# Kernel optimization log

Hardware: AMD Instinct MI355X
Metric: run time of the kernel (lower is better)

The kernel has to match this reference:

```python
import jax, jax.numpy as jnp
import numpy as np

EPS = 1e-5
NEG_SLOPE = 0.2


def _minmax(a):
    m = jnp.min(a)
    return (a - m) / (jnp.max(a) - m)


def _bn(x2d, gamma, beta):
    # train-mode BatchNorm1d: stats over axis 0 (biased variance)
    mu = x2d.mean(0)
    var = x2d.var(0)
    return gamma * (x2d - mu) * jax.lax.rsqrt(var + EPS) + beta


def _leaky(a):
    return jnp.where(a >= 0, a, NEG_SLOPE * a)


def setup_inputs() -> dict:
    key = jax.random.key(0)
    ks = jax.random.split(key, 10)
    B, C, N = 256, 1024, 80
    stdv = 1.0 / np.sqrt(C)
    return {
        "x": jax.random.normal(ks[0], (B, C, N), jnp.float32),
        "out1": jax.random.normal(ks[1], (B, N), jnp.float32),
        "adj_param": jax.random.uniform(ks[2], (N, N), jnp.float32),
        "static_weight": jax.random.uniform(ks[3], (C, C), jnp.float32, -stdv, stdv),
        "dynamic_weight": jax.random.uniform(ks[4], (C, C), jnp.float32, -stdv, stdv),
        "conv_global_w": jax.random.normal(ks[5], (C, C), jnp.float32) * 0.02,
        "conv_global_b": jnp.zeros((C,), jnp.float32),
        "conv_co_w": jax.random.normal(ks[6], (N, 2 * C), jnp.float32) * 0.02,
        "conv_co_b": jnp.zeros((N,), jnp.float32),
        "bn_gamma": jnp.ones((C,), jnp.float32),
        "bn_beta": jnp.zeros((C,), jnp.float32),
        "bng_gamma": jnp.ones((C,), jnp.float32),
        "bng_beta": jnp.zeros((C,), jnp.float32),
    }


def reference(x, out1, adj_param, static_weight, dynamic_weight,
              conv_global_w, conv_global_b, conv_co_w, conv_co_b,
              bn_gamma, bn_beta, bng_gamma, bng_beta):
    B, C, N = x.shape

    # ---- static GCN ----
    sadj = _minmax(adj_param)                               # (N,N)
    D = jax.lax.rsqrt(sadj.sum(1))                          # A.sum(1)^-0.5
    adj = D[:, None] * sadj.T * D[None, :]                  # gen_adj, diag matmuls as broadcast
    support = jnp.einsum('bcn,co->bno', x, static_weight)   # (B,N,C)
    h = jnp.einsum('nm,bmo->bno', adj, support)             # (B,N,C)
    h = _bn(h.reshape(-1, C), bn_gamma, bn_beta).reshape(B, N, C)
    out_static = _leaky(h).transpose(0, 2, 1)               # (B,C,N)
    x2 = x + out_static

    # ---- dynamic graph construction ----
    glb = x2.mean(2)                                        # GAP over nodes -> (B,C)
    glb = glb @ conv_global_w.T + conv_global_b             # 1x1 conv
    glb = _leaky(_bn(glb, bng_gamma, bng_beta))             # BN over batch (L=1)
    cat = jnp.concatenate([jnp.broadcast_to(glb[:, :, None], (B, C, N)), x2], axis=1)  # (B,2C,N)
    dadj = jnp.einsum('oc,bcn->bon', conv_co_w, cat) + conv_co_b[None, :, None]        # (B,N,N)
    dadj = _minmax(dadj)

    # ---- adjacency loss ----
    t1 = jnp.einsum('bn,bnm->bm', out1, dadj) / N
    loss = jnp.sum(jnp.linalg.norm(out1 - t1, axis=1))
    loss = loss + jnp.sum(jnp.linalg.norm((dadj - sadj).reshape(B, -1), axis=1))

    # ---- dynamic GCN ----
    Dd = jax.lax.rsqrt(dadj.sum(2))                         # (B,N)
    tadj = Dd[:, :, None] * dadj.transpose(0, 2, 1) * Dd[:, None, :]
    sup = jnp.einsum('bcn,co->bno', x2, dynamic_weight)
    h2 = jnp.einsum('bnm,bmo->bno', tadj, sup)
    h2 = _bn(h2.reshape(-1, C), bn_gamma, bn_beta).reshape(B, N, C).transpose(0, 2, 1)
    h2 = _leaky(h2)                                         # (B,C,N)
    return h2, loss
```

## Files before the change

### kernel.cpp

```cpp
#include <hip/hip_runtime.h>
#include <hip/hip_bf16.h>
#include <math.h>

#define TPB 256

constexpr int   B_  = 256;
constexpr int   C_  = 1024;
constexpr int   N_  = 80;
constexpr int   BNr = B_ * N_;
constexpr int   CN  = C_ * N_;
constexpr long  BCN = (long)B_ * C_ * N_;
constexpr int   NN  = N_ * N_;
constexpr int   BNN = B_ * NN;
constexpr float EPSf = 1e-5f;

typedef __bf16 bf16x8 __attribute__((ext_vector_type(8)));
typedef float  f32x4  __attribute__((ext_vector_type(4)));

__device__ __forceinline__ float leakyf(float v) { return v >= 0.0f ? v : 0.2f * v; }

__device__ __forceinline__ ushort f2bf(float f) {
  __hip_bfloat16 h = __float2bfloat16(f);
  ushort u; __builtin_memcpy(&u, &h, 2); return u;
}
__device__ __forceinline__ float b2f(ushort u) {
  __hip_bfloat16 h; __builtin_memcpy(&h, &u, 2);
  return __bfloat162float(h);
}

#define GLOBAL_AS __attribute__((address_space(1)))
#define LDS_AS    __attribute__((address_space(3)))
__device__ __forceinline__ void load_lds16(const void* g, void* l) {
  __builtin_amdgcn_global_load_lds((const GLOBAL_AS void*)g, (LDS_AS void*)l, 16, 0, 0);
}

__global__ __launch_bounds__(256) void k_prep_all(
    const float* __restrict__ Ws, const float* __restrict__ Wd,
    const float* __restrict__ Wco, const float* __restrict__ Wg,
    ushort* __restrict__ Wts, ushort* __restrict__ Wtd,
    ushort* __restrict__ Wco1t, ushort* __restrict__ Wco2t, ushort* __restrict__ Wg_bf,
    float* __restrict__ zbase,
    const float* __restrict__ ap, float* __restrict__ sadj,
    ushort* __restrict__ adj_bf, float* __restrict__ lossa) {
  __shared__ float sh[NN];
  __shared__ float red[TPB];
  __shared__ float sD[N_];
  __shared__ float s_lo, s_hi;
  const int t = threadIdx.x;
  const int blk = blockIdx.x;
  if (blk < 2048) {
    const float* W = (blk < 1024) ? Ws : Wd;
    ushort* Wt = (blk < 1024) ? Wts : Wtd;
    const int bb = blk & 1023;
    const int bx = bb & 31, by = bb >> 5;
    const int tx = t % 32, ty = t / 32;
    const int r0 = by * 32, c0 = bx * 32;
#pragma unroll
    for (int k = 0; k < 4; ++k) sh[(ty + 8 * k) * 33 + tx] = W[(size_t)(r0 + ty + 8 * k) * C_ + c0 + tx];
    __syncthreads();
#pragma unroll
    for (int k = 0; k < 4; ++k) Wt[(size_t)(c0 + ty + 8 * k) * C_ + r0 + tx] = f2bf(sh[tx * 33 + ty + 8 * k]);
  } else if (blk < 2208) {
    const int i4 = ((blk - 2048) * TPB + t) * 4;
    const int o = i4 >> 11, k = i4 & 2047;
    float4 v = *(const float4*)&Wco[(size_t)o * 2048 + k];
    ushort4 u;
    u.x = f2bf(v.x); u.y = f2bf(v.y); u.z = f2bf(v.z); u.w = f2bf(v.w);
    if (k < C_) *(ushort4*)&Wco1t[(size_t)o * C_ + k] = u;
    else        *(ushort4*)&Wco2t[(size_t)o * C_ + (k - C_)] = u;
  } else if (blk < 3232) {
    const long i4 = ((long)(blk - 2208) * TPB + t) * 4;
    float4 v = *(const float4*)&Wg[i4];
    ushort4 u;
    u.x = f2bf(v.x); u.y = f2bf(v.y); u.z = f2bf(v.z); u.w = f2bf(v.w);
    *(ushort4*)&Wg_bf[i4] = u;
  } else if (blk < 3258) {
    const int i = ((blk - 3232) * TPB + t) * 4;
    float4 z = make_float4(0.f, 0.f, 0.f, 0.f);
    *(float4*)&zbase[i] = z;
  } else {
    float lo = 3.4e38f, hi = -3.4e38f;
    for (int i = t; i < NN; i += TPB) { float v = ap[i]; sh[i] = v; lo = fminf(lo, v); hi = fmaxf(hi, v); }
    red[t] = lo; __syncthreads();
    for (int o = 128; o > 0; o >>= 1) { if (t < o) red[t] = fminf(red[t], red[t + o]); __syncthreads(); }
    if (t == 0) s_lo = red[0];
    __syncthreads();
    red[t] = hi; __syncthreads();
    for (int o = 128; o > 0; o >>= 1) { if (t < o) red[t] = fmaxf(red[t], red[t + o]); __syncthreads(); }
    if (t == 0) s_hi = red[0];
    __syncthreads();
    const float inv = 1.0f / (s_hi - s_lo);
    for (int i = t; i < NN; i += TPB) { float v = (sh[i] - s_lo) * inv; sh[i] = v; sadj[i] = v; }
    __syncthreads();
    if (t < N_) { float sum = 0.f; for (int m = 0; m < N_; ++m) sum += sh[t * N_ + m]; sD[t] = rsqrtf(sum); }
    if (t == 0) *lossa = 0.0f;
    __syncthreads();
    for (int i = t; i < N_ * 96; i += TPB) {
      const int n = i / 96, m = i % 96;
      adj_bf[i] = f2bf((m < N_) ? sD[n] * sh[m * N_ + n] * sD[m] : 0.0f);
    }
  }
}

__global__ __launch_bounds__(256) void k_fold_mfma(const float* __restrict__ Xf32,
                                                   const ushort* __restrict__ Xbf,
                                                   const void* __restrict__ adjsrc,
                                                   ushort* __restrict__ outp, int mode,
                                                   const float* __restrict__ bmin,
                                                   const float* __restrict__ bmax) {
  __shared__ __align__(16) ushort sX[128][104];
  __shared__ __align__(16) ushort sAdj[80][104];
  __shared__ float sD[N_];
  __shared__ float rl[TPB], rh[TPB];
  __shared__ float s_lo, s_inv;
  const int t = threadIdx.x;
  const int b  = blockIdx.x >> 3;
  const int c0 = (blockIdx.x & 7) * 128;

  if (mode == 0) {
    const ushort* ab = (const ushort*)adjsrc;
    for (int i = t; i < (N_ * 96) / 4; i += TPB) {
      ushort4 v = *(const ushort4*)&ab[i * 4];
      *(ushort4*)&sAdj[(i * 4) / 96][(i * 4) % 96] = v;
    }
    __syncthreads();
  } else {
    rl[t] = (t < 160) ? bmin[t] : 3.4e38f;
    rh[t] = (t < 160) ? bmax[t] : -3.4e38f;
    __syncthreads();
    for (int o = 128; o > 0; o >>= 1) {
      if (t < o) { rl[t] = fminf(rl[t], rl[t + o]); rh[t] = fmaxf(rh[t], rh[t + o]); }
      __syncthreads();
    }
    if (t == 0) { s_lo = rl[0]; s_inv = 1.0f / (rh[0] - rl[0]); }
    __syncthreads();
    const float lo = s_lo, inv = s_inv;
    float* sF = (float*)&sX[0][0];
    const float* db = (const float*)adjsrc + (size_t)b * NN;
    for (int i = t; i < NN / 4; i += TPB) {
      float4 v = *(const float4*)&db[i * 4];
      v.x = (v.x - lo) * inv; v.y = (v.y - lo) * inv;
      v.z = (v.z - lo) * inv; v.w = (v.w - lo) * inv;
      *(float4*)&sF[i * 4] = v;
    }
    __syncthreads();
    if (t < N_) { float s = 0.f; for (int m = 0; m < N_; ++m) s += sF[t * N_ + m]; sD[t] = rsqrtf(s); }
    __syncthreads();
    for (int i = t; i < N_ * 96; i += TPB) {
      const int n = i / 96, m = i % 96;
      sAdj[n][m] = f2bf((m < N_) ? sF[m * N_ + n] * sD[n] * sD[m] : 0.0f);
    }
    __syncthreads();
  }

  if (mode == 0) {
    const float* Xb = Xf32 + ((size_t)b * C_ + c0) * N_;
    for (int i = t; i < (128 * N_) / 4; i += TPB) {
      float4 v = *(const float4*)&Xb[i * 4];
      const int r = (i * 4) / N_, m = (i * 4) % N_;
      ushort4 u; u.x = f2bf(v.x); u.y = f2bf(v.y); u.z = f2bf(v.z); u.w = f2bf(v.w);
      *(ushort4*)&sX[r][m] = u;
    }
  } else {
    const ushort* Xb = Xbf + ((size_t)b * C_ + c0) * N_;
    for (int i = t; i < (128 * N_) / 8; i += TPB) {
      const int r = i / 10, m = (i % 10) * 8;
      uint4 v = *(const uint4*)&Xb[(size_t)r * N_ + m];
      *(uint4*)&sX[r][m] = v;
    }
  }
  for (int i = t; i < (128 * 16) / 4; i += TPB) {
    const int r = i / 4, m = 80 + (i % 4) * 4;
    ushort4 z; z.x = 0; z.y = 0; z.z = 0; z.w = 0;
    *(ushort4*)&sX[r][m] = z;
  }
  __syncthreads();

  const int lane = t & 63, wid = t >> 6;
  const int l16 = lane & 15, lq = lane >> 4;
  f32x4 acc[2][5];
#pragma unroll
  for (int i = 0; i < 2; ++i)
#pragma unroll
    for (int j = 0; j < 5; ++j) { f32x4 z = {0.f, 0.f, 0.f, 0.f}; acc[i][j] = z; }
  bf16x8 af[2][3], bfr[5][3];
#pragma unroll
  for (int i = 0; i < 2; ++i)
#pragma unroll
    for (int kk = 0; kk < 3; ++kk)
      af[i][kk] = *(const bf16x8*)&sX[wid * 32 + i * 16 + l16][kk * 32 + lq * 8];
#pragma unroll
  for (int j = 0; j < 5; ++j)
#pragma unroll
    for (int kk = 0; kk < 3; ++kk)
      bfr[j][kk] = *(const bf16x8*)&sAdj[j * 16 + l16][kk * 32 + lq * 8];
#pragma unroll
  for (int i = 0; i < 2; ++i)
#pragma unroll
    for (int j = 0; j < 5; ++j)
#pragma unroll
      for (int kk = 0; kk < 3; ++kk)
        acc[i][j] = __builtin_amdgcn_mfma_f32_16x16x32_bf16(af[i][kk], bfr[j][kk], acc[i][j], 0, 0, 0);

  ushort* ob = outp + (size_t)b * CN;
#pragma unroll
  for (int i = 0; i < 2; ++i) {
    const int c = c0 + wid * 32 + i * 16 + lq * 4;
#pragma unroll
    for (int j = 0; j < 5; ++j) {
      const int n = j * 16 + l16;
      ushort4 u;
      u.x = f2bf(acc[i][j][0]); u.y = f2bf(acc[i][j][1]);
      u.z = f2bf(acc[i][j][2]); u.w = f2bf(acc[i][j][3]);
      *(ushort4*)&ob[(size_t)n * C_ + c] = u;
    }
  }
}

__global__ __launch_bounds__(512, 2) void k_gemm_256(const ushort* __restrict__ A,
                                                     const ushort* __restrict__ Bt,
                                                     void* __restrict__ outp, int out_bf,
                                                     float* __restrict__ bnsum,
                                                     float* __restrict__ bnsq) {
  __shared__ ushort sA[2][256 * 64];
  __shared__ ushort sB[2][256 * 64];
  const int t = threadIdx.x;
  const int lane = t & 63, wid = t >> 6;
  const int wm = wid >> 2, wn = wid & 3;
  const int l16 = lane & 15, lq = lane >> 4;

  const int lin = blockIdx.x;
  const int xcd = lin & 7, bi = lin >> 3;
  const int tm = xcd * 10 + (bi >> 2);
  const int tn = bi & 3;
  const int m0 = tm * 256, o0 = tn * 256;

  const int srow = t >> 3;
  const int sswz = ((t & 7) ^ ((t >> 3) & 7)) * 8;

  f32x4 acc[8][4];
#pragma unroll
  for (int i = 0; i < 8; ++i)
#pragma unroll
    for (int j = 0; j < 4; ++j) { f32x4 z = {0.f, 0.f, 0.f, 0.f}; acc[i][j] = z; }

  bf16x8 afr[4][2], bfr0[2][2], bfr1[2][2];

#define STA(PAR, ROWB, KT) load_lds16(A  + (size_t)(m0 + (ROWB) + srow) * C_ + (KT) * 64 + sswz, \
                                      &sA[PAR][((ROWB) + (wid << 3)) * 64])
#define STB(PAR, ROWB, KT) load_lds16(Bt + (size_t)(o0 + (ROWB) + srow) * C_ + (KT) * 64 + sswz, \
                                      &sB[PAR][((ROWB) + (wid << 3)) * 64])
#define STA_H(PAR, H, KT) { STA(PAR, (H)*128, KT); STA(PAR, (H)*128 + 64, KT); }
#define STB_H(PAR, H, KT) { STB(PAR, (H)*128, KT); STB(PAR, (H)*128 + 64, KT); }

#define RDA(PAR, MH)                                                                      \
  _Pragma("unroll") for (int fi = 0; fi < 4; ++fi) {                                      \
    const int row = ((MH) ? 128 : 0) + wm * 64 + fi * 16 + l16;                           \
    _Pragma("unroll") for (int kk = 0; kk < 2; ++kk)                                      \
      afr[fi][kk] = *(const bf16x8*)&sA[PAR][row * 64 + ((kk * 4 + lq) ^ (l16 & 7)) * 8]; \
  }
#define RDB(PAR, NH, DST)                                                                 \
  _Pragma("unroll") for (int gi = 0; gi < 2; ++gi) {                                      \
    const int row = ((NH) ? 128 : 0) + wn * 32 + gi * 16 + l16;                           \
    _Pragma("unroll") for (int kk = 0; kk < 2; ++kk)                                      \
      DST[gi][kk] = *(const bf16x8*)&sB[PAR][row * 64 + ((kk * 4 + lq) ^ (l16 & 7)) * 8]; \
  }

#define MFMAS(MH, NH, BF)                                                          \
  _Pragma("unroll") for (int kk = 0; kk < 2; ++kk)                                 \
  _Pragma("unroll") for (int fi = 0; fi < 4; ++fi)                                 \
  _Pragma("unroll") for (int gi = 0; gi < 2; ++gi)                                 \
    acc[(MH) * 4 + fi][(NH) * 2 + gi] = __builtin_amdgcn_mfma_f32_16x16x32_bf16(   \
        afr[fi][kk], BF[gi][kk], acc[(MH) * 4 + fi][(NH) * 2 + gi], 0, 0, 0);

#define PHASE(MH, NH, BF, RD, STAGES, VMW)                                         \
  {                                                                                \
    RD                                                                             \
    STAGES                                                                         \
    asm volatile("s_barrier" ::: "memory");                                        \
    asm volatile("s_waitcnt lgkmcnt(0)" ::: "memory");                             \
    __builtin_amdgcn_s_setprio(1);                                                 \
    MFMAS(MH, NH, BF)                                                              \
    __builtin_amdgcn_s_setprio(0);                                                 \
    VMW                                                                            \
    asm volatile("s_barrier" ::: "memory");                                        \
  }

  STA_H(0, 0, 0); STA_H(0, 1, 0); STB_H(0, 0, 0); STB_H(0, 1, 0);
  STA_H(1, 0, 1); STB_H(1, 1, 1);
  asm volatile("s_waitcnt vmcnt(4)" ::: "memory");
  asm volatile("s_barrier" ::: "memory");

  for (int i = 0; i < 7; ++i) {
    const int t1 = 2 * i + 1, t2 = 2 * i + 2, t3 = 2 * i + 3;
    PHASE(0, 0, bfr0, RDA(0, 0) RDB(0, 0, bfr0), { STA_H(1, 1, t1); }, {})
    PHASE(0, 1, bfr1, RDB(0, 1, bfr1),           { STB_H(1, 0, t1); }, {})
    PHASE(1, 1, bfr1, RDA(0, 1),                 { STA_H(0, 0, t2); }, {})
    PHASE(1, 0, bfr0, {},                        { STB_H(0, 1, t2); }, { asm volatile("s_waitcnt vmcnt(4)" ::: "memory"); })
    PHASE(0, 0, bfr0, RDA(1, 0) RDB(1, 0, bfr0), { STA_H(0, 1, t2); }, {})
    PHASE(0, 1, bfr1, RDB(1, 1, bfr1),           { STB_H(0, 0, t2); }, {})
    PHASE(1, 1, bfr1, RDA(1, 1),                 { STA_H(1, 0, t3); }, {})
    PHASE(1, 0, bfr0, {},                        { STB_H(1, 1, t3); }, { asm volatile("s_waitcnt vmcnt(4)" ::: "memory"); })
  }
  PHASE(0, 0, bfr0, RDA(0, 0) RDB(0, 0, bfr0), { STA_H(1, 1, 15); }, {})
  PHASE(0, 1, bfr1, RDB(0, 1, bfr1),           { STB_H(1, 0, 15); }, {})
  PHASE(1, 1, bfr1, RDA(0, 1),                 {}, {})
  PHASE(1, 0, bfr0, {},                        {}, { asm volatile("s_waitcnt vmcnt(0)" ::: "memory"); })
  PHASE(0, 0, bfr0, RDA(1, 0) RDB(1, 0, bfr0), {}, {})
  PHASE(0, 1, bfr1, RDB(1, 1, bfr1),           {}, {})
  PHASE(1, 1, bfr1, RDA(1, 1),                 {}, {})
  PHASE(1, 0, bfr0, {},                        {}, {})

#pragma unroll
  for (int f = 0; f < 8; ++f) {
    const int gmb = (f < 4) ? (wm * 64 + f * 16) : (128 + wm * 64 + (f - 4) * 16);
    const int mg = m0 + gmb + lq * 4;
    const int b  = mg / 80;
    const int n0 = mg - b * 80;
#pragma unroll
    for (int gi = 0; gi < 4; ++gi) {
      const int gnb = (gi < 2) ? (wn * 32 + gi * 16) : (128 + wn * 32 + (gi - 2) * 16);
      const int og = o0 + gnb + l16;
      const size_t off = (size_t)b * CN + (size_t)og * N_ + n0;
      if (out_bf) {
        ushort4 u;
        u.x = f2bf(acc[f][gi][0]); u.y = f2bf(acc[f][gi][1]);
        u.z = f2bf(acc[f][gi][2]); u.w = f2bf(acc[f][gi][3]);
        *(ushort4*)((ushort*)outp + off) = u;
      } else {
        *(f32x4*)((float*)outp + off) = acc[f][gi];
      }
    }
  }

  {
    float* redS = (float*)&sA[0][0];
    float* redQ = redS + 2048;
    const int slot = wm * 4 + lq;
#pragma unroll
    for (int gi = 0; gi < 4; ++gi) {
      float s = 0.f, q = 0.f;
#pragma unroll
      for (int f = 0; f < 8; ++f)
#pragma unroll
        for (int r = 0; r < 4; ++r) { const float v = acc[f][gi][r]; s += v; q += v * v; }
      const int gnb = (gi < 2) ? (wn * 32 + gi * 16) : (128 + wn * 32 + (gi - 2) * 16);
      const int ol = gnb + l16;
      redS[ol * 8 + slot] = s;
      redQ[ol * 8 + slot] = q;
    }
    __syncthreads();
    if (t < 256) {
      float s = 0.f, q = 0.f;
#pragma unroll
      for (int k = 0; k < 8; ++k) { s += redS[t * 8 + k]; q += redQ[t * 8 + k]; }
      atomicAdd(&bnsum[o0 + t], s);
      atomicAdd(&bnsq[o0 + t], q);
    }
  }
#undef STA
#undef STB
#undef STA_H
#undef STB_H
#undef RDA
#undef RDB
#undef MFMAS
#undef PHASE
}

__global__ __launch_bounds__(256) void k_dadj_mfma(const ushort* __restrict__ A,
                                                   const ushort* __restrict__ Bw,
                                                   const float* __restrict__ go,
                                                   const float* __restrict__ bco,
                                                   float* __restrict__ dadj,
                                                   float* __restrict__ bmin,
                                                   float* __restrict__ bmax) {
  __shared__ ushort smA[128 * 32];
  __shared__ ushort smB[80 * 32];
  const int t = threadIdx.x;
  const int lane = t & 63, wid = t >> 6;
  const int m0 = blockIdx.x * 128;
  const int rto = t >> 2, ch = t & 3;
  const size_t gA0 = (size_t)(m0 + rto) * C_ + (size_t)ch * 8;
  ushort* ldsA = smA + wid * 512;
  const int l16 = lane & 15, lq = lane >> 4;
  const int wrow = wid * 32;
  f32x4 zero = {0.f, 0.f, 0.f, 0.f};
  f32x4 acc[2][5];
#pragma unroll
  for (int i = 0; i < 2; ++i)
#pragma unroll
    for (int j = 0; j < 5; ++j) acc[i][j] = zero;
  for (int k0 = 0; k0 < C_; k0 += 32) {
    load_lds16(A + gA0 + k0,            ldsA);
    load_lds16(A + gA0 + 64 * C_ + k0,  ldsA + 2048);
    {
      const int idx = t;
      uint4 v = *(const uint4*)&Bw[(size_t)(idx >> 2) * C_ + k0 + (idx & 3) * 8];
      *(uint4*)&smB[idx * 8] = v;
      if (t < 64) {
        const int idx2 = 256 + t;
        uint4 v2 = *(const uint4*)&Bw[(size_t)(idx2 >> 2) * C_ + k0 + (idx2 & 3) * 8];
        *(uint4*)&smB[idx2 * 8] = v2;
      }
    }
    __syncthreads();
    bf16x8 af[2], bfr[5];
#pragma unroll
    for (int i = 0; i < 2; ++i) af[i]  = *(const bf16x8*)&smA[(wrow + i * 16 + l16) * 32 + lq * 8];
#pragma unroll
    for (int j = 0; j < 5; ++j) bfr[j] = *(const bf16x8*)&smB[(j * 16 + l16) * 32 + lq * 8];
#pragma unroll
    for (int i = 0; i < 2; ++i)
#pragma unroll
      for (int j = 0; j < 5; ++j)
        acc[i][j] = __builtin_amdgcn_mfma_f32_16x16x32_bf16(af[i], bfr[j], acc[i][j], 0, 0, 0);
    __syncthreads();
  }
  float vlo = 3.4e38f, vhi = -3.4e38f;
#pragma unroll
  for (int i = 0; i < 2; ++i) {
    const int mg = m0 + wrow + i * 16 + lq * 4;
    const int b  = mg / 80;
    const int n0 = mg - b * 80;
    const float* gob = go + b * N_;
#pragma unroll
    for (int j = 0; j < 5; ++j) {
      const int o = j * 16 + l16;
      const float g = gob[o] + bco[o];
      f32x4 v = acc[i][j];
      v[0] += g; v[1] += g; v[2] += g; v[3] += g;
      vlo = fminf(vlo, fminf(fminf(v[0], v[1]), fminf(v[2], v[3])));
      vhi = fmaxf(vhi, fmaxf(fmaxf(v[0], v[1]), fmaxf(v[2], v[3])));
      *(f32x4*)&dadj[(size_t)b * NN + (size_t)o * N_ + n0] = v;
    }
  }
  float* red = (float*)smA;
  red[t] = vlo; red[TPB + t] = vhi;
  __syncthreads();
  for (int o = 128; o > 0; o >>= 1) {
    if (t < o) {
      red[t] = fminf(red[t], red[t + o]);
      red[TPB + t] = fmaxf(red[TPB + t], red[TPB + t + o]);
    }
    __syncthreads();
  }
  if (t == 0) { bmin[blockIdx.x] = red[0]; bmax[blockIdx.x] = red[TPB]; }
}

__global__ __launch_bounds__(256) void k_glb_mfma(const ushort* __restrict__ A,
                                                  const ushort* __restrict__ Bw,
                                                  const float* __restrict__ bias,
                                                  float* __restrict__ outp,
                                                  float* __restrict__ gsum,
                                                  float* __restrict__ gsq) {
  __shared__ ushort smA[2][64 * 32];
  __shared__ ushort smB[2][64 * 32];
  const int t = threadIdx.x;
  const int lane = t & 63, wid = t >> 6;
  const int o0 = blockIdx.x * 64, m0 = blockIdx.y * 64;
  const int rto = t >> 2, ch = t & 3;
  const size_t gA0 = (size_t)(m0 + rto) * C_ + (size_t)ch * 8;
  const size_t gB0 = (size_t)(o0 + rto) * C_ + (size_t)ch * 8;
  const int l16 = lane & 15, lq = lane >> 4;
  const int wm = wid & 1, wn = wid >> 1;
  f32x4 zero = {0.f, 0.f, 0.f, 0.f};
  f32x4 acc[2][2];
#pragma unroll
  for (int i = 0; i < 2; ++i)
#pragma unroll
    for (int j = 0; j < 2; ++j) acc[i][j] = zero;
  for (int k0 = 0; k0 < C_; k0 += 64) {
    load_lds16(A  + gA0 + k0,       smA[0] + wid * 512);
    load_lds16(A  + gA0 + k0 + 32,  smA[1] + wid * 512);
    load_lds16(Bw + gB0 + k0,       smB[0] + wid * 512);
    load_lds16(Bw + gB0 + k0 + 32,  smB[1] + wid * 512);
    __syncthreads();
#pragma unroll
    for (int h = 0; h < 2; ++h) {
      bf16x8 af[2], bfr[2];
#pragma unroll
      for (int i = 0; i < 2; ++i) af[i]  = *(const bf16x8*)&smA[h][(wm * 32 + i * 16 + l16) * 32 + lq * 8];
#pragma unroll
      for (int j = 0; j < 2; ++j) bfr[j] = *(const bf16x8*)&smB[h][(wn * 32 + j * 16 + l16) * 32 + lq * 8];
#pragma unroll
      for (int i = 0; i < 2; ++i)
#pragma unroll
        for (int j = 0; j < 2; ++j)
          acc[i][j] = __builtin_amdgcn_mfma_f32_16x16x32_bf16(af[i], bfr[j], acc[i][j], 0, 0, 0);
    }
    __syncthreads();
  }
  float ssv[2] = {0.f, 0.f}, sqv[2] = {0.f, 0.f};
#pragma unroll
  for (int i = 0; i < 2; ++i) {
    const int mg = m0 + wm * 32 + i * 16 + lq * 4;
#pragma unroll
    for (int j = 0; j < 2; ++j) {
      const int og = o0 + wn * 32 + j * 16 + l16;
      const float bs = bias[og];
      f32x4 v = acc[i][j];
#pragma unroll
      for (int r = 0; r < 4; ++r) {
        const float val = v[r] + bs;
        outp[(size_t)(mg + r) * C_ + og] = val;
        ssv[j] += val; sqv[j] += val * val;
      }
    }
  }
  {
    float* redS = (float*)&smA[0][0];
    float* redQ = redS + 512;
    const int slot = wm * 4 + lq;
#pragma unroll
    for (int j = 0; j < 2; ++j) {
      const int ol = wn * 32 + j * 16 + l16;
      redS[ol * 8 + slot] = ssv[j];
      redQ[ol * 8 + slot] = sqv[j];
    }
    __syncthreads();
    if (t < 64) {
      float s = 0.f, q = 0.f;
#pragma unroll
      for (int k = 0; k < 8; ++k) { s += redS[t * 8 + k]; q += redQ[t * 8 + k]; }
      atomicAdd(&gsum[o0 + t], s);
      atomicAdd(&gsq[o0 + t], q);
    }
  }
}

__global__ __launch_bounds__(256) void k_go_mfma(const float* __restrict__ glb1,
                                                 const ushort* __restrict__ Bw,
                                                 const float* __restrict__ gsum,
                                                 const float* __restrict__ gsq,
                                                 const float* __restrict__ gg,
                                                 const float* __restrict__ gb,
                                                 float* __restrict__ go) {
  __shared__ ushort smA[128 * 32];
  __shared__ ushort smB[80 * 32];
  __shared__ float pgm[C_], pmu[C_], pgb[C_];
  const int t = threadIdx.x;
  const int lane = t & 63, wid = t >> 6;
  const int kbase = blockIdx.x * 128;
  const int m0 = blockIdx.y * 128;
  const int rto = t >> 2, ch = t & 3;
  const int l16 = lane & 15, lq = lane >> 4;
  const int wrow = wid * 32;
  for (int c = t; c < C_; c += TPB) {
    const float mu = gsum[c] * (1.0f / B_);
    const float var = gsq[c] * (1.0f / B_) - mu * mu;
    pgm[c] = gg[c] * rsqrtf(var + EPSf); pmu[c] = mu; pgb[c] = gb[c];
  }
  __syncthreads();
  f32x4 zero = {0.f, 0.f, 0.f, 0.f};
  f32x4 acc[2][5];
#pragma unroll
  for (int i = 0; i < 2; ++i)
#pragma unroll
    for (int j = 0; j < 5; ++j) acc[i][j] = zero;
  for (int kk0 = 0; kk0 < 128; kk0 += 32) {
    const int k0 = kbase + kk0;
#pragma unroll
    for (int h = 0; h < 2; ++h) {
      const float* src = &glb1[(size_t)(m0 + h * 64 + rto) * C_ + k0 + ch * 8];
      float4 a0 = *(const float4*)src;
      float4 a1 = *(const float4*)(src + 4);
      float av[8] = {a0.x, a0.y, a0.z, a0.w, a1.x, a1.y, a1.z, a1.w};
      ushort4 u0, u1;
      const int cb = k0 + ch * 8;
      u0.x = f2bf(leakyf(pgm[cb+0]*(av[0]-pmu[cb+0])+pgb[cb+0]));
      u0.y = f2bf(leakyf(pgm[cb+1]*(av[1]-pmu[cb+1])+pgb[cb+1]));
      u0.z = f2bf(leakyf(pgm[cb+2]*(av[2]-pmu[cb+2])+pgb[cb+2]));
      u0.w = f2bf(leakyf(pgm[cb+3]*(av[3]-pmu[cb+3])+pgb[cb+3]));
      u1.x = f2bf(leakyf(pgm[cb+4]*(av[4]-pmu[cb+4])+pgb[cb+4]));
      u1.y = f2bf(leakyf(pgm[cb+5]*(av[5]-pmu[cb+5])+pgb[cb+5]));
      u1.z = f2bf(leakyf(pgm[cb+6]*(av[6]-pmu[cb+6])+pgb[cb+6]));
      u1.w = f2bf(leakyf(pgm[cb+7]*(av[7]-pmu[cb+7])+pgb[cb+7]));
      *(ushort4*)&smA[h * 2048 + t * 8]     = u0;
      *(ushort4*)&smA[h * 2048 + t * 8 + 4] = u1;
    }
    {
      const int idx = t;
      uint4 v = *(const uint4*)&Bw[(size_t)(idx >> 2) * C_ + k0 + (idx & 3) * 8];
      *(uint4*)&smB[idx * 8] = v;
      if (t < 64) {
        const int idx2 = 256 + t;
        uint4 v2 = *(const uint4*)&Bw[(size_t)(idx2 >> 2) * C_ + k0 + (idx2 & 3) * 8];
        *(uint4*)&smB[idx2 * 8] = v2;
      }
    }
    __syncthreads();
    bf16x8 af[2], bfr[5];
#pragma unroll
    for (int i = 0; i < 2; ++i) af[i]  = *(const bf16x8*)&smA[(wrow + i * 16 + l16) * 32 + lq * 8];
#pragma unroll
    for (int j = 0; j < 5; ++j) bfr[j] = *(const bf16x8*)&smB[(j * 16 + l16) * 32 + lq * 8];
#pragma unroll
    for (int i = 0; i < 2; ++i)
#pragma unroll
      for (int j = 0; j < 5; ++j)
        acc[i][j] = __builtin_amdgcn_mfma_f32_16x16x32_bf16(af[i], bfr[j], acc[i][j], 0, 0, 0);
    __syncthreads();
  }
#pragma unroll
  for (int i = 0; i < 2; ++i) {
    const int mg = m0 + wrow + i * 16 + lq * 4;
#pragma unroll
    for (int j = 0; j < 5; ++j) {
      const int o = j * 16 + l16;
#pragma unroll
      for (int r = 0; r < 4; ++r)
        atomicAdd(&go[(size_t)(mg + r) * N_ + o], acc[i][j][r]);
    }
  }
}

__global__ __launch_bounds__(256) void k_x2_fused(
    const float* __restrict__ x, ushort* __restrict__ hx,
    const float* __restrict__ g, const float* __restrict__ be,
    const float* __restrict__ ssum, const float* __restrict__ ssq,
    ushort* __restrict__ x2t, ushort* __restrict__ glb0b) {
  __shared__ float s[64][85];
  __shared__ float pg[64], pm[64], pb[64];
  const int t = threadIdx.x;
  const long row0 = (long)blockIdx.x * 64;
  const int b = (int)(row0 >> 10), c0 = (int)(row0 & 1023);
  if (t < 64) {
    const int c = c0 + t;
    const float mu = ssum[c] * (1.0f / BNr);
    const float var = ssq[c] * (1.0f / BNr) - mu * mu;
    const float rstd = rsqrtf(var + EPSf);
    pg[t] = g[c] * rstd; pm[t] = mu; pb[t] = be[c];
  }
  __syncthreads();
  const float* xb = x  + row0 * N_;
  ushort*      hb = hx + row0 * N_;
  for (int i4 = t; i4 < (64 * N_) / 4; i4 += TPB) {
    const int e = i4 * 4, r = e / N_, n = e % N_;
    float4 xv = *(const float4*)&xb[e];
    ushort4 hu = *(const ushort4*)&hb[e];
    const float gm = pg[r], m = pm[r], bb = pb[r];
    float4 o;
    o.x = xv.x + leakyf(gm * (b2f(hu.x) - m) + bb);
    o.y = xv.y + leakyf(gm * (b2f(hu.y) - m) + bb);
    o.z = xv.z + leakyf(gm * (b2f(hu.z) - m) + bb);
    o.w = xv.w + leakyf(gm * (b2f(hu.w) - m) + bb);
    *(float4*)&s[r][n] = o;
    ushort4 ou;
    ou.x = f2bf(o.x); ou.y = f2bf(o.y); ou.z = f2bf(o.z); ou.w = f2bf(o.w);
    *(ushort4*)&hb[e] = ou;
  }
  __syncthreads();
  const int tx = t % 16, ty = t / 16;
  ushort* tb = x2t + (size_t)b * CN + c0 + tx * 4;
#pragma unroll
  for (int u = 0; u < 5; ++u) {
    const int n = ty + 16 * u;
    ushort4 v;
    v.x = f2bf(s[tx * 4 + 0][n]); v.y = f2bf(s[tx * 4 + 1][n]);
    v.z = f2bf(s[tx * 4 + 2][n]); v.w = f2bf(s[tx * 4 + 3][n]);
    *(ushort4*)&tb[(size_t)n * C_] = v;
  }
  {
    const int r = t >> 2, q = t & 3;
    float sacc = 0.f;
    for (int n = q; n < N_; n += 4) sacc += s[r][n];
    sacc += __shfl_down(sacc, 1);
    sacc += __shfl_down(sacc, 2);
    if (q == 0) glb0b[(size_t)b * C_ + c0 + r] = f2bf(sacc * (1.0f / N_));
  }
}

__global__ void k_loss(const float* __restrict__ dadj, const float* __restrict__ sadj,
                       const float* __restrict__ out1, float* __restrict__ lossa,
                       const float* __restrict__ bmin, const float* __restrict__ bmax) {
  const int b = blockIdx.x, t = threadIdx.x;
  __shared__ float red[TPB], red2[TPB];
  __shared__ float slo, sinv, s2;
  red[t]  = (t < 160) ? bmin[t] : 3.4e38f;
  red2[t] = (t < 160) ? bmax[t] : -3.4e38f;
  __syncthreads();
  for (int o = 128; o > 0; o >>= 1) {
    if (t < o) { red[t] = fminf(red[t], red[t + o]); red2[t] = fmaxf(red2[t], red2[t + o]); }
    __syncthreads();
  }
  if (t == 0) { slo = red[0]; sinv = 1.0f / (red2[0] - red[0]); }
  __syncthreads();
  const float lo = slo, inv = sinv;
  const float* db = dadj + (long)b * NN;
  const float* o1 = out1 + b * N_;
  float p2 = 0.f;
  for (int i = t; i < NN; i += TPB) { const float d = (db[i] - lo) * inv - sadj[i]; p2 += d * d; }
  float p1 = 0.f;
  if (t < N_) {
    float acc = 0.f;
    for (int n = 0; n < N_; ++n) acc += o1[n] * ((db[n * N_ + t] - lo) * inv);
    const float d = o1[t] - acc * (1.0f / N_);
    p1 = d * d;
  }
  red[t] = p2; __syncthreads();
  for (int o = 128; o > 0; o >>= 1) { if (t < o) red[t] += red[t + o]; __syncthreads(); }
  if (t == 0) s2 = red[0];
  __syncthreads();
  red[t] = p1; __syncthreads();
  for (int o = 128; o > 0; o >>= 1) { if (t < o) red[t] += red[t + o]; __syncthreads(); }
  if (t == 0) atomicAdd(lossa, sqrtf(s2) + sqrtf(red[0]));
}

__global__ void k_final(const ushort* __restrict__ h2, float* __restrict__ outp,
                        const float* __restrict__ g, const float* __restrict__ be,
                        const float* __restrict__ ssum, const float* __restrict__ ssq,
                        const float* __restrict__ lossa) {
  const long i = ((long)blockIdx.x * TPB + threadIdx.x) * 4;
  const int c = (int)((i / N_) % C_);
  ushort4 hu = *(const ushort4*)&h2[i];
  const float mu = ssum[c] * (1.0f / BNr);
  const float rstd = rsqrtf(ssq[c] * (1.0f / BNr) - mu * mu + EPSf);
  const float gm = g[c] * rstd, bb = be[c];
  float4 v;
  v.x = leakyf(gm * (b2f(hu.x) - mu) + bb);
  v.y = leakyf(gm * (b2f(hu.y) - mu) + bb);
  v.z = leakyf(gm * (b2f(hu.z) - mu) + bb);
  v.w = leakyf(gm * (b2f(hu.w) - mu) + bb);
  *(float4*)&outp[i] = v;
  if (blockIdx.x == 0 && threadIdx.x == 0) outp[BCN] = *lossa;
}

extern "C" void kernel_launch(void* const* d_in, const int* in_sizes, int n_in,
                              void* d_out, int out_size, void* d_ws, size_t ws_size,
                              hipStream_t stream) {
  const float* x    = (const float*)d_in[0];
  const float* out1 = (const float*)d_in[1];
  const float* ap   = (const float*)d_in[2];
  const float* Ws   = (const float*)d_in[3];
  const float* Wd   = (const float*)d_in[4];
  const float* Wg   = (const float*)d_in[5];
  const float* bg   = (const float*)d_in[6];
  const float* Wco  = (const float*)d_in[7];
  const float* bco  = (const float*)d_in[8];
  const float* bn_g  = (const float*)d_in[9];
  const float* bn_b  = (const float*)d_in[10];
  const float* bng_g = (const float*)d_in[11];
  const float* bng_b = (const float*)d_in[12];
  float* out = (float*)d_out;

  float* w = (float*)d_ws;
  float* sadj  = w;
  float* dadj  = sadj + NN;
  float* glb0  = dadj + BNN;
  float* glb1  = glb0 + B_ * C_;
  float* go    = glb1 + B_ * C_;
  float* ssum1 = go + BNr;
  float* ssq1  = ssum1 + C_;
  float* ssum2 = ssq1 + C_;
  float* ssq2  = ssum2 + C_;
  float* gsum  = ssq2 + C_;
  float* gsq   = gsum + C_;
  float* bmin  = gsq + C_;
  float* bmax  = bmin + 512;
  float* lossa = bmax + 512;
  ushort* ub   = (ushort*)(((uintptr_t)(lossa + 1) + 255) & ~(uintptr_t)255);
  ushort* xa_bf  = ub;
  ushort* hT_bf  = xa_bf + BCN;
  ushort* Wts    = hT_bf + BCN;
  ushort* Wtd    = Wts + (size_t)C_ * C_;
  ushort* Wco2t  = Wtd + (size_t)C_ * C_;
  ushort* adj_bf = Wco2t + (size_t)N_ * C_;
  ushort* Wg_bf   = (ushort*)dadj;
  ushort* Wco1t   = (ushort*)dadj + (size_t)C_ * C_;
  ushort* glb0_bf = (ushort*)glb0;
  ushort* x2t_bf  = xa_bf;

  k_prep_all<<<3259, TPB, 0, stream>>>(Ws, Wd, Wco, Wg, Wts, Wtd, Wco1t, Wco2t, Wg_bf,
                                       go, ap, sadj, adj_bf, lossa);

  k_fold_mfma<<<B_ * 8, TPB, 0, stream>>>(x, hT_bf, adj_bf, xa_bf, 0, bmin, bmax);
  k_gemm_256<<<320, 512, 0, stream>>>(xa_bf, Wts, hT_bf, 1, ssum1, ssq1);
  k_x2_fused<<<(B_ * C_) / 64, TPB, 0, stream>>>(x, hT_bf, bn_g, bn_b, ssum1, ssq1,
                                                 x2t_bf, glb0_bf);

  k_glb_mfma<<<dim3(C_ / 64, B_ / 64), TPB, 0, stream>>>(glb0_bf, Wg_bf, bg, glb1, gsum, gsq);
  k_go_mfma<<<dim3(8, B_ / 128), TPB, 0, stream>>>(glb1, Wco1t, gsum, gsq, bng_g, bng_b, go);
  k_dadj_mfma<<<BNr / 128, TPB, 0, stream>>>(x2t_bf, Wco2t, go, bco, dadj, bmin, bmax);

  k_loss<<<B_, TPB, 0, stream>>>(dadj, sadj, out1, lossa, bmin, bmax);

  k_fold_mfma<<<B_ * 8, TPB, 0, stream>>>(x, hT_bf, dadj, xa_bf, 1, bmin, bmax);
  k_gemm_256<<<320, 512, 0, stream>>>(xa_bf, Wtd, hT_bf, 1, ssum2, ssq2);
  k_final<<<(int)(BCN / (4 * TPB)), TPB, 0, stream>>>(hT_bf, out, bn_g, bn_b, ssum2, ssq2, lossa);
}
```

Before: 501.2 us.

## Retile big GEMM to 320x128 tiles with 512 blocks

Replaces the 256x256 output tile GEMM (320 blocks) with a 320x128 tile GEMM launched as 512 blocks. 512 blocks divide evenly over the 256 CUs, whereas 320 left a partial second wave. The simpler pipeline stages a whole k-tile per step and waits with vmcnt(0), so the earlier finer-grained overlap of global loads with MFMAs is reduced. Each block also does less reuse per loaded byte, and the BN-stat reduction is resized to 16 slots and 128 columns.

```diff
diff --git a/kernel.cpp b/kernel.cpp
--- a/kernel.cpp
+++ b/kernel.cpp
@@ -217,118 +217,91 @@
   }
 }
 
-__global__ __launch_bounds__(512, 2) void k_gemm_256(const ushort* __restrict__ A,
+__global__ __launch_bounds__(512, 2) void k_gemm_320(const ushort* __restrict__ A,
                                                      const ushort* __restrict__ Bt,
                                                      void* __restrict__ outp, int out_bf,
                                                      float* __restrict__ bnsum,
                                                      float* __restrict__ bnsq) {
-  __shared__ ushort sA[2][256 * 64];
-  __shared__ ushort sB[2][256 * 64];
+  __shared__ ushort sA[2][320 * 64];
+  __shared__ ushort sB[2][128 * 64];
   const int t = threadIdx.x;
   const int lane = t & 63, wid = t >> 6;
-  const int wm = wid >> 2, wn = wid & 3;
+  const int wm = wid >> 1, wn = wid & 1;
   const int l16 = lane & 15, lq = lane >> 4;
 
   const int lin = blockIdx.x;
   const int xcd = lin & 7, bi = lin >> 3;
-  const int tm = xcd * 10 + (bi >> 2);
-  const int tn = bi & 3;
-  const int m0 = tm * 256, o0 = tn * 256;
+  const int tm = xcd * 8 + (bi >> 3);
+  const int tn = bi & 7;
+  const int m0 = tm * 320, o0 = tn * 128;
 
   const int srow = t >> 3;
   const int sswz = ((t & 7) ^ ((t >> 3) & 7)) * 8;
 
-  f32x4 acc[8][4];
-#pragma unroll
-  for (int i = 0; i < 8; ++i)
+  f32x4 acc[5][4];
+#pragma unroll
+  for (int i = 0; i < 5; ++i)
 #pragma unroll
     for (int j = 0; j < 4; ++j) { f32x4 z = {0.f, 0.f, 0.f, 0.f}; acc[i][j] = z; }
-
-  bf16x8 afr[4][2], bfr0[2][2], bfr1[2][2];
 
 #define STA(PAR, ROWB, KT) load_lds16(A  + (size_t)(m0 + (ROWB) + srow) * C_ + (KT) * 64 + sswz, \
                                       &sA[PAR][((ROWB) + (wid << 3)) * 64])
 #define STB(PAR, ROWB, KT) load_lds16(Bt + (size_t)(o0 + (ROWB) + srow) * C_ + (KT) * 64 + sswz, \
                                       &sB[PAR][((ROWB) + (wid << 3)) * 64])
-#define STA_H(PAR, H, KT) { STA(PAR, (H)*128, KT); STA(PAR, (H)*128 + 64, KT); }
-#define STB_H(PAR, H, KT) { STB(PAR, (H)*128, KT); STB(PAR, (H)*128 + 64, KT); }
-
-#define RDA(PAR, MH)                                                                      \
-  _Pragma("unroll") for (int fi = 0; fi < 4; ++fi) {                                      \
-    const int row = ((MH) ? 128 : 0) + wm * 64 + fi * 16 + l16;                           \
-    _Pragma("unroll") for (int kk = 0; kk < 2; ++kk)                                      \
-      afr[fi][kk] = *(const bf16x8*)&sA[PAR][row * 64 + ((kk * 4 + lq) ^ (l16 & 7)) * 8]; \
-  }
-#define RDB(PAR, NH, DST)                                                                 \
-  _Pragma("unroll") for (int gi = 0; gi < 2; ++gi) {                                      \
-    const int row = ((NH) ? 128 : 0) + wn * 32 + gi * 16 + l16;                           \
-    _Pragma("unroll") for (int kk = 0; kk < 2; ++kk)                                      \
-      DST[gi][kk] = *(const bf16x8*)&sB[PAR][row * 64 + ((kk * 4 + lq) ^ (l16 & 7)) * 8]; \
-  }
-
-#define MFMAS(MH, NH, BF)                                                          \
-  _Pragma("unroll") for (int kk = 0; kk < 2; ++kk)                                 \
-  _Pragma("unroll") for (int fi = 0; fi < 4; ++fi)                                 \
-  _Pragma("unroll") for (int gi = 0; gi < 2; ++gi)                                 \
-    acc[(MH) * 4 + fi][(NH) * 2 + gi] = __builtin_amdgcn_mfma_f32_16x16x32_bf16(   \
-        afr[fi][kk], BF[gi][kk], acc[(MH) * 4 + fi][(NH) * 2 + gi], 0, 0, 0);
-
-#define PHASE(MH, NH, BF, RD, STAGES, VMW)                                         \
-  {                                                                                \
-    RD                                                                             \
-    STAGES                                                                         \
-    asm volatile("s_barrier" ::: "memory");                                        \
-    asm volatile("s_waitcnt lgkmcnt(0)" ::: "memory");                             \
-    __builtin_amdgcn_s_setprio(1);                                                 \
-    MFMAS(MH, NH, BF)                                                              \
-    __builtin_amdgcn_s_setprio(0);                                                 \
-    VMW                                                                            \
-    asm volatile("s_barrier" ::: "memory");                                        \
-  }
-
-  STA_H(0, 0, 0); STA_H(0, 1, 0); STB_H(0, 0, 0); STB_H(0, 1, 0);
-  STA_H(1, 0, 1); STB_H(1, 1, 1);
-  asm volatile("s_waitcnt vmcnt(4)" ::: "memory");
+#define STAGE_T(PAR, KT) { STA(PAR, 0, KT); STA(PAR, 64, KT); STA(PAR, 128, KT); \
+                           STA(PAR, 192, KT); STA(PAR, 256, KT); \
+                           STB(PAR, 0, KT); STB(PAR, 64, KT); }
+
+#define PH(PAR, KK, STAGES, VMW)                                                          \
+  {                                                                                       \
+    STAGES                                                                                \
+    bf16x8 afr[5], bfr[4];                                                                \
+    _Pragma("unroll") for (int fi = 0; fi < 5; ++fi)                                      \
+      afr[fi] = *(const bf16x8*)&sA[PAR][(wm * 80 + fi * 16 + l16) * 64 +                 \
+                                         (((KK) * 4 + lq) ^ (l16 & 7)) * 8];              \
+    _Pragma("unroll") for (int gi = 0; gi < 4; ++gi)                                      \
+      bfr[gi] = *(const bf16x8*)&sB[PAR][(wn * 64 + gi * 16 + l16) * 64 +                 \
+                                         (((KK) * 4 + lq) ^ (l16 & 7)) * 8];              \
+    asm volatile("s_barrier" ::: "memory");                                               \
+    asm volatile("s_waitcnt lgkmcnt(0)" ::: "memory");                                    \
+    __builtin_amdgcn_s_setprio(1);                                                        \
+    _Pragma("unroll") for (int fi = 0; fi < 5; ++fi)                                      \
+      _Pragma("unroll") for (int gi = 0; gi < 4; ++gi)                                    \
+        acc[fi][gi] = __builtin_amdgcn_mfma_f32_16x16x32_bf16(afr[fi], bfr[gi],           \
+                                                              acc[fi][gi], 0, 0, 0);      \
+    __builtin_amdgcn_s_setprio(0);                                                        \
+    VMW                                                                                   \
+    asm volatile("s_barrier" ::: "memory");                                               \
+  }
+
+  STAGE_T(0, 0);
+  asm volatile("s_waitcnt vmcnt(0)" ::: "memory");
   asm volatile("s_barrier" ::: "memory");
 
-  for (int i = 0; i < 7; ++i) {
-    const int t1 = 2 * i + 1, t2 = 2 * i + 2, t3 = 2 * i + 3;
-    PHASE(0, 0, bfr0, RDA(0, 0) RDB(0, 0, bfr0), { STA_H(1, 1, t1); }, {})
-    PHASE(0, 1, bfr1, RDB(0, 1, bfr1),           { STB_H(1, 0, t1); }, {})
-    PHASE(1, 1, bfr1, RDA(0, 1),                 { STA_H(0, 0, t2); }, {})
-    PHASE(1, 0, bfr0, {},                        { STB_H(0, 1, t2); }, { asm volatile("s_waitcnt vmcnt(4)" ::: "memory"); })
-    PHASE(0, 0, bfr0, RDA(1, 0) RDB(1, 0, bfr0), { STA_H(0, 1, t2); }, {})
-    PHASE(0, 1, bfr1, RDB(1, 1, bfr1),           { STB_H(0, 0, t2); }, {})
-    PHASE(1, 1, bfr1, RDA(1, 1),                 { STA_H(1, 0, t3); }, {})
-    PHASE(1, 0, bfr0, {},                        { STB_H(1, 1, t3); }, { asm volatile("s_waitcnt vmcnt(4)" ::: "memory"); })
-  }
-  PHASE(0, 0, bfr0, RDA(0, 0) RDB(0, 0, bfr0), { STA_H(1, 1, 15); }, {})
-  PHASE(0, 1, bfr1, RDB(0, 1, bfr1),           { STB_H(1, 0, 15); }, {})
-  PHASE(1, 1, bfr1, RDA(0, 1),                 {}, {})
-  PHASE(1, 0, bfr0, {},                        {}, { asm volatile("s_waitcnt vmcnt(0)" ::: "memory"); })
-  PHASE(0, 0, bfr0, RDA(1, 0) RDB(1, 0, bfr0), {}, {})
-  PHASE(0, 1, bfr1, RDB(1, 1, bfr1),           {}, {})
-  PHASE(1, 1, bfr1, RDA(1, 1),                 {}, {})
-  PHASE(1, 0, bfr0, {},                        {}, {})
-
-#pragma unroll
-  for (int f = 0; f < 8; ++f) {
-    const int gmb = (f < 4) ? (wm * 64 + f * 16) : (128 + wm * 64 + (f - 4) * 16);
-    const int mg = m0 + gmb + lq * 4;
+  for (int i = 0; i < 8; ++i) {
+    const int t1 = 2 * i + 1, t2 = 2 * i + 2;
+    PH(0, 0, { STAGE_T(1, t1); }, {})
+    PH(0, 1, {}, { asm volatile("s_waitcnt vmcnt(0)" ::: "memory"); })
+    PH(1, 0, { if (i < 7) STAGE_T(0, t2); }, {})
+    PH(1, 1, {}, { if (i < 7) { asm volatile("s_waitcnt vmcnt(0)" ::: "memory"); } })
+  }
+
+#pragma unroll
+  for (int fi = 0; fi < 5; ++fi) {
+    const int mg = m0 + wm * 80 + fi * 16 + lq * 4;
     const int b  = mg / 80;
     const int n0 = mg - b * 80;
 #pragma unroll
     for (int gi = 0; gi < 4; ++gi) {
-      const int gnb = (gi < 2) ? (wn * 32 + gi * 16) : (128 + wn * 32 + (gi - 2) * 16);
-      const int og = o0 + gnb + l16;
+      const int og = o0 + wn * 64 + gi * 16 + l16;
       const size_t off = (size_t)b * CN + (size_t)og * N_ + n0;
       if (out_bf) {
         ushort4 u;
-        u.x = f2bf(acc[f][gi][0]); u.y = f2bf(acc[f][gi][1]);
-        u.z = f2bf(acc[f][gi][2]); u.w = f2bf(acc[f][gi][3]);
+        u.x = f2bf(acc[fi][gi][0]); u.y = f2bf(acc[fi][gi][1]);
+        u.z = f2bf(acc[fi][gi][2]); u.w = f2bf(acc[fi][gi][3]);
         *(ushort4*)((ushort*)outp + off) = u;
       } else {
-        *(f32x4*)((float*)outp + off) = acc[f][gi];
+        *(f32x4*)((float*)outp + off) = acc[fi][gi];
       }
     }
   }
@@ -341,31 +314,26 @@
     for (int gi = 0; gi < 4; ++gi) {
       float s = 0.f, q = 0.f;
 #pragma unroll
-      for (int f = 0; f < 8; ++f)
-#pragma unroll
-        for (int r = 0; r < 4; ++r) { const float v = acc[f][gi][r]; s += v; q += v * v; }
-      const int gnb = (gi < 2) ? (wn * 32 + gi * 16) : (128 + wn * 32 + (gi - 2) * 16);
-      const int ol = gnb + l16;
-      redS[ol * 8 + slot] = s;
-      redQ[ol * 8 + slot] = q;
-    }
-    __syncthreads();
-    if (t < 256) {
+      for (int fi = 0; fi < 5; ++fi)
+#pragma unroll
+        for (int r = 0; r < 4; ++r) { const float v = acc[fi][gi][r]; s += v; q += v * v; }
+      const int ol = wn * 64 + gi * 16 + l16;
+      redS[ol * 16 + slot] = s;
+      redQ[ol * 16 + slot] = q;
+    }
+    __syncthreads();
+    if (t < 128) {
       float s = 0.f, q = 0.f;
 #pragma unroll
-      for (int k = 0; k < 8; ++k) { s += redS[t * 8 + k]; q += redQ[t * 8 + k]; }
+      for (int k = 0; k < 16; ++k) { s += redS[t * 16 + k]; q += redQ[t * 16 + k]; }
       atomicAdd(&bnsum[o0 + t], s);
       atomicAdd(&bnsq[o0 + t], q);
     }
   }
 #undef STA
 #undef STB
-#undef STA_H
-#undef STB_H
-#undef RDA
-#undef RDB
-#undef MFMAS
-#undef PHASE
+#undef STAGE_T
+#undef PH
 }
 
 __global__ __launch_bounds__(256) void k_dadj_mfma(const ushort* __restrict__ A,
@@ -775,7 +743,7 @@
                                        go, ap, sadj, adj_bf, lossa);
 
   k_fold_mfma<<<B_ * 8, TPB, 0, stream>>>(x, hT_bf, adj_bf, xa_bf, 0, bmin, bmax);
-  k_gemm_256<<<320, 512, 0, stream>>>(xa_bf, Wts, hT_bf, 1, ssum1, ssq1);
+  k_gemm_320<<<512, 512, 0, stream>>>(xa_bf, Wts, hT_bf, 1, ssum1, ssq1);
   k_x2_fused<<<(B_ * C_) / 64, TPB, 0, stream>>>(x, hT_bf, bn_g, bn_b, ssum1, ssq1,
                                                  x2t_bf, glb0_bf);
 
@@ -786,6 +754,6 @@
   k_loss<<<B_, TPB, 0, stream>>>(dadj, sadj, out1, lossa, bmin, bmax);
 
   k_fold_mfma<<<B_ * 8, TPB, 0, stream>>>(x, hT_bf, dadj, xa_bf, 1, bmin, bmax);
-  k_gemm_256<<<320, 512, 0, stream>>>(xa_bf, Wtd, hT_bf, 1, ssum2, ssq2);
+  k_gemm_320<<<512, 512, 0, stream>>>(xa_bf, Wtd, hT_bf, 1, ssum2, ssq2);
   k_final<<<(int)(BCN / (4 * TPB)), TPB, 0, stream>>>(hT_bf, out, bn_g, bn_b, ssum2, ssq2, lossa);
 }
```

Measured after the change: 491.4 us. Within noise of the previous version (-2.0%).
